# Optimization experiments

Measured on AMD Instinct MI355X. Metric: run time of the kernel, lower is better.

Reference implementation:

```python
import jax, jax.numpy as jnp
import numpy as np

B, N, FIN, FOUT, H = 8, 1024, 256, 256, 4
D = FOUT // H  # head_dim = 64
LN_EPS = 1e-5
NEG_INF = -1e9


def setup_inputs() -> dict:
    key = jax.random.key(0)
    k_x, k_adj, k_w, k_a = jax.random.split(key, 4)
    x = jax.random.normal(k_x, (B, N, FIN), dtype=jnp.float32)
    # sparse binary adjacency with self-loops (dense mask, as the module expects)
    adj = (jax.random.uniform(k_adj, (B, N, N)) < 0.05).astype(jnp.float32)
    adj = jnp.maximum(adj, jnp.eye(N, dtype=jnp.float32)[None])
    W = jax.random.normal(k_w, (FIN, FOUT), dtype=jnp.float32) * 0.02
    gamma = jnp.ones((FOUT,), dtype=jnp.float32)
    beta = jnp.zeros((FOUT,), dtype=jnp.float32)
    a = jax.random.normal(k_a, (2 * D,), dtype=jnp.float32) * 0.02
    return {"x": x, "adj_matrix": adj, "W": W, "gamma": gamma, "beta": beta, "a": a}


def reference(x, adj_matrix, W, gamma, beta, a):
    # h = LayerNorm(x @ W)
    h = jnp.einsum("bnf,fo->bno", x, W)
    mu = jnp.mean(h, axis=-1, keepdims=True)
    var = jnp.mean(jnp.square(h - mu), axis=-1, keepdims=True)
    h = (h - mu) * jax.lax.rsqrt(var + LN_EPS) * gamma + beta
    h = h.reshape(B, N, H, D)
    # a^T [h_i ; h_j] == a_src . h_i + a_dst . h_j  (exact decomposition of the
    # concat+Linear(2D->1) attention score, avoiding the O(B*N^2*H*2D) concat)
    a_src, a_dst = a[:D], a[D:]
    e_i = jnp.einsum("bnhd,d->bnh", h, a_src)  # term for node i (query)
    e_j = jnp.einsum("bnhd,d->bnh", h, a_dst)  # term for node j (key)
    e = e_i[:, :, None, :] + e_j[:, None, :, :]  # [B, N_i, N_j, H]
    e = jnp.where(e > 0, e, 0.2 * e)  # LeakyReLU(0.2)
    e = jnp.where(adj_matrix[..., None] == 0, NEG_INF, e)
    alpha = jax.nn.softmax(e, axis=2)  # softmax over neighbors j
    # dropout is identity in eval/reference mode
    h_out = jnp.einsum("bijh,bjhd->bihd", alpha, h)
    return h_out.reshape(B, N, FOUT)
```

## Files before the change

### kernel.cpp

```cpp
#include <hip/hip_runtime.h>
#include <hip/hip_bf16.h>

#define BB 8
#define NN 1024
#define FIN 256
#define FOUT 256
#define NH 4
#define CAP 192

typedef short short8 __attribute__((ext_vector_type(8)));
typedef short short4v __attribute__((ext_vector_type(4)));
typedef float floatx4 __attribute__((ext_vector_type(4)));

__device__ __forceinline__ short f2bf(float f) {
    unsigned int u = __builtin_bit_cast(unsigned int, f);
    unsigned int r = (u + 0x7fffu + ((u >> 16) & 1u)) >> 16;
    return (short)r;
}
__device__ __forceinline__ float bf2f(unsigned short s) {
    return __builtin_bit_cast(float, (unsigned int)s << 16);
}

__global__ __launch_bounds__(256) void k_wt(const float* __restrict__ W,
                                            unsigned short* __restrict__ Wt) {
    __shared__ unsigned short ts[64][80];
    const int k0 = blockIdx.x * 64, n0 = blockIdx.y * 64;
    const int t = threadIdx.x;
#pragma unroll
    for (int q = 0; q < 4; ++q) {
        int lin = t + q * 256;
        int r = lin >> 4, c4 = lin & 15;
        float4 v = *(const float4*)&W[(size_t)(k0 + r) * FOUT + n0 + c4 * 4];
        ts[c4 * 4 + 0][r] = (unsigned short)f2bf(v.x);
        ts[c4 * 4 + 1][r] = (unsigned short)f2bf(v.y);
        ts[c4 * 4 + 2][r] = (unsigned short)f2bf(v.z);
        ts[c4 * 4 + 3][r] = (unsigned short)f2bf(v.w);
    }
    __syncthreads();
#pragma unroll
    for (int q = 0; q < 2; ++q) {
        int lin = t + q * 256;
        int row = lin >> 3, kg = lin & 7;
        short8 s = *(short8*)&ts[row][kg * 8];
        *(short8*)&Wt[(size_t)(n0 + row) * FIN + k0 + kg * 8] = s;
    }
}

__global__ __launch_bounds__(256) void k_gemm_ln(const float* __restrict__ x,
                                                 const unsigned short* __restrict__ Wt,
                                                 const float* __restrict__ gamma,
                                                 const float* __restrict__ beta,
                                                 const float* __restrict__ a,
                                                 unsigned short* __restrict__ hb,
                                                 float* __restrict__ e_src,
                                                 float* __restrict__ e_dst) {
    __shared__ unsigned short As[16 * 264];
    __shared__ float sumL[4][16], sqL[4][16];
    const int m0 = blockIdx.x * 16;
    const int t = threadIdx.x;
    const int w = t >> 6, lane = t & 63, quad = lane >> 4, l15 = lane & 15;

#pragma unroll
    for (int q = 0; q < 4; ++q) {
        int lin = t + q * 256;
        int row = lin >> 6, c4 = lin & 63;
        float4 v = *(const float4*)&x[(size_t)(m0 + row) * FIN + c4 * 4];
        short4v s;
        s.x = f2bf(v.x); s.y = f2bf(v.y); s.z = f2bf(v.z); s.w = f2bf(v.w);
        *(short4v*)&As[row * 264 + c4 * 4] = s;
    }
    __syncthreads();

    floatx4 acc[4];
#pragma unroll
    for (int nt = 0; nt < 4; ++nt) acc[nt] = (floatx4)0.f;

#pragma unroll
    for (int ks = 0; ks < 8; ++ks) {
        short8 af = *(short8*)&As[l15 * 264 + ks * 32 + quad * 8];
#pragma unroll
        for (int nt = 0; nt < 4; ++nt) {
            short8 bf = *(const short8*)&Wt[(size_t)((w * 4 + nt) * 16 + l15) * FIN + ks * 32 + quad * 8];
            acc[nt] = __builtin_amdgcn_mfma_f32_16x16x32_bf16(af, bf, acc[nt], 0, 0, 0);
        }
    }

    float rs[4], rq[4];
#pragma unroll
    for (int reg = 0; reg < 4; ++reg) {
        float s = 0.f, q2 = 0.f;
#pragma unroll
        for (int nt = 0; nt < 4; ++nt) { float v = acc[nt][reg]; s += v; q2 = fmaf(v, v, q2); }
#pragma unroll
        for (int off = 1; off < 16; off <<= 1) { s += __shfl_xor(s, off); q2 += __shfl_xor(q2, off); }
        rs[reg] = s; rq[reg] = q2;
    }
    if (l15 == 0) {
#pragma unroll
        for (int reg = 0; reg < 4; ++reg) {
            sumL[w][quad * 4 + reg] = rs[reg];
            sqL[w][quad * 4 + reg] = rq[reg];
        }
    }
    __syncthreads();

    float g[4], bt[4], as_[4], ad_[4];
#pragma unroll
    for (int nt = 0; nt < 4; ++nt) {
        int col = w * 64 + nt * 16 + l15;
        g[nt] = gamma[col]; bt[nt] = beta[col];
        int d = nt * 16 + l15;
        as_[nt] = a[d]; ad_[nt] = a[64 + d];
    }

    float pes[4], ped[4];
#pragma unroll
    for (int reg = 0; reg < 4; ++reg) {
        int row = quad * 4 + reg;
        float mean = (sumL[0][row] + sumL[1][row] + sumL[2][row] + sumL[3][row]) * (1.f / 256.f);
        float msq  = (sqL[0][row] + sqL[1][row] + sqL[2][row] + sqL[3][row]) * (1.f / 256.f);
        float inv = rsqrtf(msq - mean * mean + 1e-5f);
        float es = 0.f, ed = 0.f;
#pragma unroll
        for (int nt = 0; nt < 4; ++nt) {
            float hn = (acc[nt][reg] - mean) * inv * g[nt] + bt[nt];
            As[row * 264 + w * 64 + nt * 16 + l15] = (unsigned short)f2bf(hn);
            es = fmaf(hn, as_[nt], es);
            ed = fmaf(hn, ad_[nt], ed);
        }
        pes[reg] = es; ped[reg] = ed;
    }
#pragma unroll
    for (int reg = 0; reg < 4; ++reg) {
#pragma unroll
        for (int off = 1; off < 16; off <<= 1) {
            pes[reg] += __shfl_xor(pes[reg], off);
            ped[reg] += __shfl_xor(ped[reg], off);
        }
    }
    if (l15 == 0) {
#pragma unroll
        for (int reg = 0; reg < 4; ++reg) {
            int rowg = m0 + quad * 4 + reg;
            e_src[rowg * NH + w] = pes[reg];
            e_dst[rowg * NH + w] = ped[reg];
        }
    }
    __syncthreads();

#pragma unroll
    for (int q = 0; q < 2; ++q) {
        int lin = t + q * 256;
        int row = lin >> 5, cg = lin & 31;
        short8 s = *(short8*)&As[row * 264 + cg * 8];
        *(short8*)&hb[(size_t)(m0 + row) * FOUT + cg * 8] = s;
    }
}

__global__ __launch_bounds__(256) void k_attn(const unsigned short* __restrict__ hb,
                                              const float* __restrict__ adj,
                                              const float* __restrict__ e_src,
                                              const float* __restrict__ e_dst,
                                              float* __restrict__ out) {
    __shared__ int cnt;
    __shared__ int jlist[CAP];
    __shared__ float4 wsl[CAP];
    __shared__ float accs[4][4][64];
    __shared__ float Ss[4][64];

    const int b = blockIdx.y;
    const int i = blockIdx.x;
    const int t = threadIdx.x;
    const int lane = t & 63;
    const int w = t >> 6;
    const unsigned short* hp = hb + (size_t)b * NN * FOUT;
    const float* adjp = adj + ((size_t)b * NN + i) * NN;
    const float* edp  = e_dst + (size_t)b * NN * NH;
    const float4 esv = *(const float4*)&e_src[((size_t)b * NN + i) * NH];

    if (t == 0) cnt = 0;
    __syncthreads();

    float4 av = *(const float4*)&adjp[t * 4];
    float am[4] = {av.x, av.y, av.z, av.w};
#pragma unroll
    for (int q = 0; q < 4; ++q) {
        bool nz = (am[q] != 0.0f);
        unsigned long long mask = __ballot(nz);
        int basew = 0;
        if (lane == 0) basew = mask ? atomicAdd(&cnt, __popcll(mask)) : 0;
        basew = __shfl(basew, 0);
        if (nz) {
            int pos = basew + __popcll(mask & ((1ull << lane) - 1ull));
            int j = t * 4 + q;
            float4 ed = *(const float4*)&edp[(size_t)j * NH];
            float e0 = esv.x + ed.x, e1 = esv.y + ed.y, e2 = esv.z + ed.z, e3 = esv.w + ed.w;
            e0 = e0 > 0.f ? e0 : 0.2f * e0;
            e1 = e1 > 0.f ? e1 : 0.2f * e1;
            e2 = e2 > 0.f ? e2 : 0.2f * e2;
            e3 = e3 > 0.f ? e3 : 0.2f * e3;
            float4 w4;
            w4.x = __expf(e0); w4.y = __expf(e1); w4.z = __expf(e2); w4.w = __expf(e3);
            jlist[pos] = j;
            wsl[pos] = w4;
        }
    }
    __syncthreads();

    const int n = cnt;
    const int fg = lane;
    const int hh = fg >> 4;
    float4 acc = make_float4(0.f, 0.f, 0.f, 0.f);
    float S = 0.f;

    int idx = w;
    while (idx + 12 < n) {
        int jj[4]; float wv[4]; short4v hv[4];
#pragma unroll
        for (int q = 0; q < 4; ++q) {
            int p = idx + 4 * q;
            jj[q] = jlist[p];
            wv[q] = ((const float*)&wsl[p])[hh];
        }
#pragma unroll
        for (int q = 0; q < 4; ++q)
            hv[q] = *(const short4v*)&hp[(size_t)jj[q] * FOUT + fg * 4];
#pragma unroll
        for (int q = 0; q < 4; ++q) {
            acc.x = fmaf(wv[q], bf2f((unsigned short)hv[q].x), acc.x);
            acc.y = fmaf(wv[q], bf2f((unsigned short)hv[q].y), acc.y);
            acc.z = fmaf(wv[q], bf2f((unsigned short)hv[q].z), acc.z);
            acc.w = fmaf(wv[q], bf2f((unsigned short)hv[q].w), acc.w);
            S += wv[q];
        }
        idx += 16;
    }
    for (; idx < n; idx += 4) {
        int j = jlist[idx];
        float wv = ((const float*)&wsl[idx])[hh];
        short4v hv = *(const short4v*)&hp[(size_t)j * FOUT + fg * 4];
        acc.x = fmaf(wv, bf2f((unsigned short)hv.x), acc.x);
        acc.y = fmaf(wv, bf2f((unsigned short)hv.y), acc.y);
        acc.z = fmaf(wv, bf2f((unsigned short)hv.z), acc.z);
        acc.w = fmaf(wv, bf2f((unsigned short)hv.w), acc.w);
        S += wv;
    }

    accs[w][0][fg] = acc.x; accs[w][1][fg] = acc.y;
    accs[w][2][fg] = acc.z; accs[w][3][fg] = acc.w;
    Ss[w][fg] = S;
    __syncthreads();

    if (t < 64) {
        float4 o = make_float4(0.f, 0.f, 0.f, 0.f);
        float St = 0.f;
#pragma unroll
        for (int q = 0; q < 4; ++q) {
            o.x += accs[q][0][t]; o.y += accs[q][1][t];
            o.z += accs[q][2][t]; o.w += accs[q][3][t];
            St += Ss[q][t];
        }
        float inv = 1.0f / St;
        o.x *= inv; o.y *= inv; o.z *= inv; o.w *= inv;
        *(float4*)&out[((size_t)b * NN + i) * FOUT + t * 4] = o;
    }
}

extern "C" void kernel_launch(void* const* d_in, const int* in_sizes, int n_in,
                              void* d_out, int out_size, void* d_ws, size_t ws_size,
                              hipStream_t stream) {
    const float* x     = (const float*)d_in[0];
    const float* adj   = (const float*)d_in[1];
    const float* W     = (const float*)d_in[2];
    const float* gamma = (const float*)d_in[3];
    const float* beta  = (const float*)d_in[4];
    const float* a     = (const float*)d_in[5];
    float* out = (float*)d_out;

    unsigned short* Wt = (unsigned short*)d_ws;
    unsigned short* hb = Wt + (size_t)FIN * FOUT;
    float* e_src = (float*)(hb + (size_t)BB * NN * FOUT);
    float* e_dst = e_src + (size_t)BB * NN * NH;

    k_wt<<<dim3(4, 4), 256, 0, stream>>>(W, Wt);
    k_gemm_ln<<<dim3(512), 256, 0, stream>>>(x, Wt, gamma, beta, a, hb, e_src, e_dst);
    k_attn<<<dim3(NN, BB), 256, 0, stream>>>(hb, adj, e_src, e_dst, out);
}
```

Before: 123.0 us.

## Assign one wavefront per attention row, dropping block-level atomics and reductions

The attention kernel now handles four query rows per block, one per wavefront. Each wavefront scans its own adjacency row with ballot and prefix popcount into a private neighbor list, so the shared atomic counter, the block barriers and the cross-wave shared-memory reduction are gone. The gather loop is unrolled to eight neighbors for more loads in flight. The tradeoff is that each row is now served by one wave instead of four, so per-row latency is longer while the grid has a quarter as many blocks.

```diff
diff --git a/kernel.cpp b/kernel.cpp
--- a/kernel.cpp
+++ b/kernel.cpp
@@ -7,6 +7,7 @@
 #define FOUT 256
 #define NH 4
 #define CAP 192
+#define RPB 4
 
 typedef short short8 __attribute__((ext_vector_type(8)));
 typedef short short4v __attribute__((ext_vector_type(4)));
@@ -162,83 +163,73 @@
                                               const float* __restrict__ e_src,
                                               const float* __restrict__ e_dst,
                                               float* __restrict__ out) {
-    __shared__ int cnt;
-    __shared__ int jlist[CAP];
-    __shared__ float4 wsl[CAP];
-    __shared__ float accs[4][4][64];
-    __shared__ float Ss[4][64];
+    __shared__ int jl[RPB][CAP];
+    __shared__ float4 wl[RPB][CAP];
 
     const int b = blockIdx.y;
-    const int i = blockIdx.x;
     const int t = threadIdx.x;
-    const int lane = t & 63;
-    const int w = t >> 6;
+    const int w = t >> 6, lane = t & 63;
+    const int i = blockIdx.x * RPB + w;
     const unsigned short* hp = hb + (size_t)b * NN * FOUT;
     const float* adjp = adj + ((size_t)b * NN + i) * NN;
     const float* edp  = e_dst + (size_t)b * NN * NH;
     const float4 esv = *(const float4*)&e_src[((size_t)b * NN + i) * NH];
-
-    if (t == 0) cnt = 0;
-    __syncthreads();
-
-    float4 av = *(const float4*)&adjp[t * 4];
-    float am[4] = {av.x, av.y, av.z, av.w};
+    const unsigned long long lmask = (1ull << lane) - 1ull;
+
+    int n = 0;
 #pragma unroll
     for (int q = 0; q < 4; ++q) {
-        bool nz = (am[q] != 0.0f);
-        unsigned long long mask = __ballot(nz);
-        int basew = 0;
-        if (lane == 0) basew = mask ? atomicAdd(&cnt, __popcll(mask)) : 0;
-        basew = __shfl(basew, 0);
-        if (nz) {
-            int pos = basew + __popcll(mask & ((1ull << lane) - 1ull));
-            int j = t * 4 + q;
-            float4 ed = *(const float4*)&edp[(size_t)j * NH];
-            float e0 = esv.x + ed.x, e1 = esv.y + ed.y, e2 = esv.z + ed.z, e3 = esv.w + ed.w;
-            e0 = e0 > 0.f ? e0 : 0.2f * e0;
-            e1 = e1 > 0.f ? e1 : 0.2f * e1;
-            e2 = e2 > 0.f ? e2 : 0.2f * e2;
-            e3 = e3 > 0.f ? e3 : 0.2f * e3;
-            float4 w4;
-            w4.x = __expf(e0); w4.y = __expf(e1); w4.z = __expf(e2); w4.w = __expf(e3);
-            jlist[pos] = j;
-            wsl[pos] = w4;
-        }
-    }
-    __syncthreads();
-
-    const int n = cnt;
-    const int fg = lane;
-    const int hh = fg >> 4;
+        float4 av = *(const float4*)&adjp[(q * 64 + lane) * 4];
+        float am[4] = {av.x, av.y, av.z, av.w};
+#pragma unroll
+        for (int c = 0; c < 4; ++c) {
+            bool nz = (am[c] != 0.0f);
+            unsigned long long m = __ballot(nz);
+            if (nz) {
+                int pos = n + __popcll(m & lmask);
+                int j = (q * 64 + lane) * 4 + c;
+                float4 ed = *(const float4*)&edp[(size_t)j * NH];
+                float e0 = esv.x + ed.x, e1 = esv.y + ed.y, e2 = esv.z + ed.z, e3 = esv.w + ed.w;
+                e0 = e0 > 0.f ? e0 : 0.2f * e0;
+                e1 = e1 > 0.f ? e1 : 0.2f * e1;
+                e2 = e2 > 0.f ? e2 : 0.2f * e2;
+                e3 = e3 > 0.f ? e3 : 0.2f * e3;
+                float4 w4;
+                w4.x = __expf(e0); w4.y = __expf(e1); w4.z = __expf(e2); w4.w = __expf(e3);
+                jl[w][pos] = j;
+                wl[w][pos] = w4;
+            }
+            n += __popcll(m);
+        }
+    }
+
+    const int hh = lane >> 4;
     float4 acc = make_float4(0.f, 0.f, 0.f, 0.f);
     float S = 0.f;
-
-    int idx = w;
-    while (idx + 12 < n) {
-        int jj[4]; float wv[4]; short4v hv[4];
-#pragma unroll
-        for (int q = 0; q < 4; ++q) {
-            int p = idx + 4 * q;
-            jj[q] = jlist[p];
-            wv[q] = ((const float*)&wsl[p])[hh];
-        }
-#pragma unroll
-        for (int q = 0; q < 4; ++q)
-            hv[q] = *(const short4v*)&hp[(size_t)jj[q] * FOUT + fg * 4];
-#pragma unroll
-        for (int q = 0; q < 4; ++q) {
+    int p = 0;
+    for (; p + 8 <= n; p += 8) {
+        int jj[8]; float wv[8]; short4v hv[8];
+#pragma unroll
+        for (int q = 0; q < 8; ++q) {
+            jj[q] = jl[w][p + q];
+            wv[q] = ((const float*)&wl[w][p + q])[hh];
+        }
+#pragma unroll
+        for (int q = 0; q < 8; ++q)
+            hv[q] = *(const short4v*)&hp[(size_t)jj[q] * FOUT + lane * 4];
+#pragma unroll
+        for (int q = 0; q < 8; ++q) {
             acc.x = fmaf(wv[q], bf2f((unsigned short)hv[q].x), acc.x);
             acc.y = fmaf(wv[q], bf2f((unsigned short)hv[q].y), acc.y);
             acc.z = fmaf(wv[q], bf2f((unsigned short)hv[q].z), acc.z);
             acc.w = fmaf(wv[q], bf2f((unsigned short)hv[q].w), acc.w);
             S += wv[q];
         }
-        idx += 16;
-    }
-    for (; idx < n; idx += 4) {
-        int j = jlist[idx];
-        float wv = ((const float*)&wsl[idx])[hh];
-        short4v hv = *(const short4v*)&hp[(size_t)j * FOUT + fg * 4];
+    }
+    for (; p < n; ++p) {
+        int j = jl[w][p];
+        float wv = ((const float*)&wl[w][p])[hh];
+        short4v hv = *(const short4v*)&hp[(size_t)j * FOUT + lane * 4];
         acc.x = fmaf(wv, bf2f((unsigned short)hv.x), acc.x);
         acc.y = fmaf(wv, bf2f((unsigned short)hv.y), acc.y);
         acc.z = fmaf(wv, bf2f((unsigned short)hv.z), acc.z);
@@ -246,24 +237,9 @@
         S += wv;
     }
 
-    accs[w][0][fg] = acc.x; accs[w][1][fg] = acc.y;
-    accs[w][2][fg] = acc.z; accs[w][3][fg] = acc.w;
-    Ss[w][fg] = S;
-    __syncthreads();
-
-    if (t < 64) {
-        float4 o = make_float4(0.f, 0.f, 0.f, 0.f);
-        float St = 0.f;
-#pragma unroll
-        for (int q = 0; q < 4; ++q) {
-            o.x += accs[q][0][t]; o.y += accs[q][1][t];
-            o.z += accs[q][2][t]; o.w += accs[q][3][t];
-            St += Ss[q][t];
-        }
-        float inv = 1.0f / St;
-        o.x *= inv; o.y *= inv; o.z *= inv; o.w *= inv;
-        *(float4*)&out[((size_t)b * NN + i) * FOUT + t * 4] = o;
-    }
+    float inv = 1.0f / S;
+    float4 o = make_float4(acc.x * inv, acc.y * inv, acc.z * inv, acc.w * inv);
+    *(float4*)&out[((size_t)b * NN + i) * FOUT + lane * 4] = o;
 }
 
 extern "C" void kernel_launch(void* const* d_in, const int* in_sizes, int n_in,
@@ -284,5 +260,5 @@
 
     k_wt<<<dim3(4, 4), 256, 0, stream>>>(W, Wt);
     k_gemm_ln<<<dim3(512), 256, 0, stream>>>(x, Wt, gamma, beta, a, hb, e_src, e_dst);
-    k_attn<<<dim3(NN, BB), 256, 0, stream>>>(hb, adj, e_src, e_dst, out);
-}
+    k_attn<<<dim3(NN / RPB, BB), 256, 0, stream>>>(hb, adj, e_src, e_dst, out);
+}
```

Measured after the change: 123.9 us. No clear change (+0.8%).
